# Kernel tuning notes

Measured on AMD Instinct MI355X. Metric: run time of the kernel, lower is better.

## Reference

```python
import jax, jax.numpy as jnp
import numpy as np

DCR = 8      # depth_channel_ratio
CLIP = 0.3   # clipping_ratio
ITER = 32    # iterative_num
EPS = 1e-6


def setup_inputs() -> dict:
    key = jax.random.key(0)
    k1, k2 = jax.random.split(key)
    B, C, H, W = 8, 128, 96, 320
    input_features = jax.random.normal(k1, (B, C, H, W), dtype=jnp.float32)
    dynamic_masks = jax.random.randint(k2, (B, H, W), 0, 2, dtype=jnp.int32)
    return {"input_features": input_features, "dynamic_masks": dynamic_masks}


def _channel_selection(x):
    # Select 2*(C//DCR) channels most similar to pseudo disparity/depth ramps.
    B, C, H, W = x.shape
    disp = jnp.linspace(0.1, 1.0, H, dtype=x.dtype)                      # (H,)
    disp_full = jnp.broadcast_to(disp[None, :, None], (B, H, W)).reshape(-1)  # (B*H*W,)
    depth_full = 1.0 - disp_full
    s = jax.nn.sigmoid(x).transpose(1, 0, 2, 3).reshape(C, -1)           # (C, B*H*W)
    sn = jnp.maximum(jnp.sqrt(jnp.sum(s * s, axis=-1)), EPS)             # (C,)

    def cos_sim(v):
        vn = jnp.maximum(jnp.sqrt(jnp.sum(v * v)), EPS)
        return (s @ v) / (sn * vn)                                       # (C,)

    nsel = C // DCR
    disp_idx = jnp.argsort(-cos_sim(disp_full))[:nsel]
    depth_idx = jnp.argsort(-cos_sim(depth_full))[:nsel]
    return jnp.concatenate([disp_idx, depth_idx])                        # (2*nsel,)


def _clip_norm(v, clip_ratio):
    # per-(batch,channel) max over spatial dims, scaled, zero->1, clamp to [0,1]
    m = jnp.max(v, axis=(2, 3), keepdims=True) * clip_ratio
    m = jnp.where(m == 0, jnp.ones_like(m), m)
    return jnp.clip(v / m, 0.0, 1.0)


def reference(input_features, dynamic_masks):
    B, C, H, W = input_features.shape
    idx = _channel_selection(input_features)
    sel = input_features[:, idx]                       # (B, ns, H, W)
    # mask resolution == feature resolution, so nearest resize is identity
    m = dynamic_masks.astype(input_features.dtype)[:, None]  # (B,1,H,W) broadcast over ns
    iters = int(ITER * H / dynamic_masks.shape[1])     # == ITER here (static)

    pad_bottom = lambda t: jnp.concatenate([t, t[:, :, -1:]], axis=2)
    prop0 = pad_bottom(sel)                            # (B, ns, H+1, W)

    def step(prop, _):
        core = m * prop[:, :, 1:] + (1.0 - m) * sel    # pull values up one row where masked
        return pad_bottom(core), None

    prop, _ = jax.lax.scan(step, prop0, None, length=iters)
    prop = prop[:, :, :-1]                             # (B, ns, H, W)

    w = _clip_norm(jnp.abs(prop - sel), CLIP)
    w = jnp.max(w, axis=1, keepdims=True)              # (B,1,H,W)
    refined = w * prop + (1.0 - w) * sel
    return input_features.at[:, idx].set(refined)
```

## Files before the change

### kernel.cpp

```cpp
#include <hip/hip_runtime.h>
#include <cstdint>
#include <cstddef>

#define BB 8
#define CC 128
#define HH 96
#define WW 320
#define HW (HH*WW)
#define NSEL 32
#define NSELH 16
#define K1CH 2
#define K4CH 8

typedef float f32x4 __attribute__((ext_vector_type(4)));

__device__ __forceinline__ float sigmoidf_(float x) {
  return __builtin_amdgcn_rcpf(1.0f + __expf(-x));
}

__global__ __launch_bounds__(256) void k_copy_reduce(
    const float* __restrict__ x, float* __restrict__ out,
    double* __restrict__ partials) {
  int t = threadIdx.x;
  int chunk = blockIdx.x & (K1CH-1);
  int bc = blockIdx.x >> 1;
  const f32x4* __restrict__ xi = (const f32x4*)(x + (size_t)bc * HW);
  f32x4* __restrict__ oi = (f32x4*)(out + (size_t)bc * HW);
  float tf = 0.0f, af = 0.0f, qf = 0.0f;
  #pragma unroll 1
  for (int outer = 0; outer < 3; ++outer) {
    int base = chunk*3840 + outer*1280;
    f32x4 v[5];
    #pragma unroll
    for (int u = 0; u < 5; u++) v[u] = xi[base + u*256 + t];
    __builtin_amdgcn_sched_barrier(0);
    #pragma unroll
    for (int u = 0; u < 5; u++) oi[base + u*256 + t] = v[u];
    #pragma unroll
    for (int u = 0; u < 5; u++) {
      int j = base + u*256 + t;
      int h = j / (WW/4);
      float d = 0.1f + (float)h * (0.9f/95.0f);
      float s0 = sigmoidf_(v[u].x), s1 = sigmoidf_(v[u].y);
      float s2 = sigmoidf_(v[u].z), s3 = sigmoidf_(v[u].w);
      float ts = (s0+s1)+(s2+s3);
      tf += ts;
      af += ts * d;
      qf += (s0*s0+s1*s1)+(s2*s2+s3*s3);
    }
  }
  __shared__ double sh[3][256];
  sh[0][t]=(double)tf; sh[1][t]=(double)af; sh[2][t]=(double)qf;
  __syncthreads();
  for (int ofs=128; ofs>0; ofs>>=1) {
    if (t < ofs) {
      sh[0][t]+=sh[0][t+ofs];
      sh[1][t]+=sh[1][t+ofs];
      sh[2][t]+=sh[2][t+ofs];
    }
    __syncthreads();
  }
  if (t==0) {
    int p = bc*K1CH + chunk;
    partials[p*3+0]=sh[0][0];
    partials[p*3+1]=sh[1][0];
    partials[p*3+2]=sh[2][0];
  }
}

__global__ __launch_bounds__(128) void k_select_runs(
    const double* __restrict__ partials, const int* __restrict__ mask,
    int* __restrict__ idx, uint8_t* __restrict__ kk) {
  int t = threadIdx.x;
  if (blockIdx.x == 0) {
    int c = t;
    double T=0.0, A=0.0, Q=0.0;
    for (int b=0;b<BB;b++) {
      for (int ch=0; ch<K1CH; ch++) {
        int p = (b*CC + c)*K1CH + ch;
        T += partials[p*3+0];
        A += partials[p*3+1];
        Q += partials[p*3+2];
      }
    }
    double sn = sqrt(Q); if (sn < 1e-6) sn = 1e-6;
    double c1 = A / sn;
    double c2 = (T - A) / sn;
    __shared__ double s1[CC], s2[CC];
    s1[c]=c1; s2[c]=c2;
    __syncthreads();
    int r1=0, r2=0;
    for (int j=0;j<CC;j++) {
      r1 += (s1[j] > c1) || (s1[j]==c1 && j<c);
      r2 += (s2[j] > c2) || (s2[j]==c2 && j<c);
    }
    if (r1 < NSELH) idx[r1] = c;
    if (r2 < NSELH) idx[NSELH + r2] = c;
  } else {
    int colid = (blockIdx.x - 1)*128 + t;
    int b = colid / WW;
    int w = colid - b*WW;
    const int* __restrict__ mcol = mask + (size_t)b*HW + w;
    unsigned long long lo=0ull, hi=0ull;
    #pragma unroll
    for (int h=0; h<64; ++h) lo |= (unsigned long long)(mcol[h*WW]!=0) << h;
    #pragma unroll
    for (int h=64; h<95; ++h) hi |= (unsigned long long)(mcol[h*WW]!=0) << (h-64);
    uint8_t* __restrict__ kcol = kk + (size_t)b*HW + w;
    #pragma unroll
    for (int h=0; h<96; ++h) {
      unsigned long long s;
      if (h == 0)      s = lo;
      else if (h < 64) s = (lo >> h) | (hi << (64-h));
      else             s = hi >> (h-64);
      int run = __builtin_ctzll(~s | (1ull<<33));
      kcol[h*WW] = (uint8_t)(run > 32 ? 32 : run);
    }
  }
}

__global__ __launch_bounds__(256) void k_maxdiff(
    const float* __restrict__ x, const int* __restrict__ idx,
    const uint8_t* __restrict__ kk, float* __restrict__ pmax) {
  int chunk = blockIdx.x & (K4CH-1);
  int bc32 = blockIdx.x >> 3;
  int b = bc32 >> 5;
  int c = bc32 & 31;
  int ic = idx[c];
  const float* __restrict__ base = x + ((size_t)b*CC + ic)*HW;
  const uint8_t* __restrict__ kb = kk + (size_t)b*HW;
  float mx = 0.0f;
  int lo = chunk * (HW/4/K4CH), hiend = lo + (HW/4/K4CH);
  for (int j = lo + threadIdx.x; j < hiend; j += 256) {
    f32x4 sel = ((const f32x4*)base)[j];
    uchar4 kv  = ((const uchar4*)kb)[j];
    int h = j / (WW/4);
    int w4 = (j - h*(WW/4))*4;
    float p0 = base[(h+(int)kv.x)*WW + w4+0];
    float p1 = base[(h+(int)kv.y)*WW + w4+1];
    float p2 = base[(h+(int)kv.z)*WW + w4+2];
    float p3 = base[(h+(int)kv.w)*WW + w4+3];
    mx = fmaxf(mx, fmaxf(fmaxf(fabsf(p0-sel.x), fabsf(p1-sel.y)),
                         fmaxf(fabsf(p2-sel.z), fabsf(p3-sel.w))));
  }
  __shared__ float sh[256];
  sh[threadIdx.x]=mx; __syncthreads();
  for (int ofs=128; ofs>0; ofs>>=1) {
    if ((int)threadIdx.x<ofs) sh[threadIdx.x]=fmaxf(sh[threadIdx.x], sh[threadIdx.x+ofs]);
    __syncthreads();
  }
  if (threadIdx.x==0) pmax[blockIdx.x] = sh[0];
}

__global__ __launch_bounds__(WW) void k_refine(
    const float* __restrict__ x, const int* __restrict__ idx,
    const uint8_t* __restrict__ kk, const float* __restrict__ pmax,
    float* __restrict__ out) {
  int bh = blockIdx.x;
  int b = bh / HH, h = bh - b*HH;
  int w = threadIdx.x;
  __shared__ int sidx[NSEL];
  __shared__ float smc[NSEL];
  if (threadIdx.x < NSEL) {
    int c = threadIdx.x;
    sidx[c] = idx[c];
    float m = 0.0f;
    #pragma unroll
    for (int ch=0; ch<K4CH; ch++) m = fmaxf(m, pmax[(b*NSEL + c)*K4CH + ch]);
    m *= 0.3f;
    if (m == 0.0f) m = 1.0f;
    smc[c] = m;
  }
  __syncthreads();
  int r = h + (int)kk[(size_t)bh*WW + w];
  float sel[NSEL], prop[NSEL];
  float wmax = 0.0f;
  #pragma unroll
  for (int c=0;c<NSEL;c++) {
    const float* __restrict__ base = x + ((size_t)b*CC + sidx[c])*HW;
    sel[c]  = base[h*WW + w];
    prop[c] = base[r*WW + w];
    float v = fabsf(prop[c]-sel[c]) / smc[c];
    wmax = fmaxf(wmax, fminf(v, 1.0f));
  }
  #pragma unroll
  for (int c=0;c<NSEL;c++) {
    float rf = wmax*prop[c] + (1.0f - wmax)*sel[c];
    out[((size_t)b*CC + sidx[c])*HW + h*WW + w] = rf;
  }
}

extern "C" void kernel_launch(void* const* d_in, const int* in_sizes, int n_in,
                              void* d_out, int out_size, void* d_ws, size_t ws_size,
                              hipStream_t stream) {
  const float* x   = (const float*)d_in[0];
  const int* mask  = (const int*)d_in[1];
  float* out       = (float*)d_out;

  char* ws = (char*)d_ws;
  double* partials = (double*)(ws);
  int*    idx      = (int*)(ws + 49152);
  float*  pmax     = (float*)(ws + 49152 + 128);
  uint8_t* kk      = (uint8_t*)(ws + 49152 + 128 + 8192);

  k_copy_reduce<<<BB*CC*K1CH, 256, 0, stream>>>(x, out, partials);
  k_select_runs<<<21, 128, 0, stream>>>(partials, mask, idx, kk);
  k_maxdiff<<<BB*NSEL*K4CH, 256, 0, stream>>>(x, idx, kk, pmax);
  k_refine<<<BB*HH, WW, 0, stream>>>(x, idx, kk, pmax, out);
}
```

Baseline: 95.72 us.

## Grid-stride copy-reduce with wave-level partial sums and separate plane reduction kernel

The copy-plus-sigmoid-statistics kernel moves from 2048 blocks each owning half a channel plane to a fixed 2048-block grid-stride loop over the whole tensor. Each wavefront reduces its partials with shuffles and writes float partials per step. A new kernel then sums those per-plane partials in double. The aim is a streaming access pattern and cheaper in-kernel reductions, paid for by an extra launch and float partial accumulation before the double sum.

```diff
diff --git a/kernel.cpp b/kernel.cpp
--- a/kernel.cpp
+++ b/kernel.cpp
@@ -9,8 +9,9 @@
 #define HW (HH*WW)
 #define NSEL 32
 #define NSELH 16
-#define K1CH 2
 #define K4CH 8
+#define GRID1 2048
+#define STEPS 15
 
 typedef float f32x4 __attribute__((ext_vector_type(4)));
 
@@ -18,70 +19,88 @@
   return __builtin_amdgcn_rcpf(1.0f + __expf(-x));
 }
 
+__device__ __forceinline__ float wred(float v) {
+  #pragma unroll
+  for (int m = 32; m >= 1; m >>= 1) v += __shfl_xor(v, m, 64);
+  return v;
+}
+
 __global__ __launch_bounds__(256) void k_copy_reduce(
     const float* __restrict__ x, float* __restrict__ out,
-    double* __restrict__ partials) {
+    float* __restrict__ wpart) {
   int t = threadIdx.x;
-  int chunk = blockIdx.x & (K1CH-1);
-  int bc = blockIdx.x >> 1;
-  const f32x4* __restrict__ xi = (const f32x4*)(x + (size_t)bc * HW);
-  f32x4* __restrict__ oi = (f32x4*)(out + (size_t)bc * HW);
-  float tf = 0.0f, af = 0.0f, qf = 0.0f;
+  int blk = blockIdx.x;
+  int wv = t >> 6;
+  const f32x4* __restrict__ xi = (const f32x4*)x;
+  f32x4* __restrict__ oi = (f32x4*)out;
   #pragma unroll 1
-  for (int outer = 0; outer < 3; ++outer) {
-    int base = chunk*3840 + outer*1280;
-    f32x4 v[5];
-    #pragma unroll
-    for (int u = 0; u < 5; u++) v[u] = xi[base + u*256 + t];
-    __builtin_amdgcn_sched_barrier(0);
-    #pragma unroll
-    for (int u = 0; u < 5; u++) oi[base + u*256 + t] = v[u];
-    #pragma unroll
-    for (int u = 0; u < 5; u++) {
-      int j = base + u*256 + t;
-      int h = j / (WW/4);
-      float d = 0.1f + (float)h * (0.9f/95.0f);
-      float s0 = sigmoidf_(v[u].x), s1 = sigmoidf_(v[u].y);
-      float s2 = sigmoidf_(v[u].z), s3 = sigmoidf_(v[u].w);
-      float ts = (s0+s1)+(s2+s3);
-      tf += ts;
-      af += ts * d;
-      qf += (s0*s0+s1*s1)+(s2*s2+s3*s3);
-    }
-  }
-  __shared__ double sh[3][256];
-  sh[0][t]=(double)tf; sh[1][t]=(double)af; sh[2][t]=(double)qf;
+  for (int s = 0; s < STEPS; ++s) {
+    int g = (s << 19) + blk*256 + t;
+    f32x4 v = xi[g];
+    oi[g] = v;
+    unsigned ip = (unsigned)g % 7680u;
+    int h = (int)(ip / 80u);
+    float d = 0.1f + (float)h * (0.9f/95.0f);
+    float s0 = sigmoidf_(v.x), s1 = sigmoidf_(v.y);
+    float s2 = sigmoidf_(v.z), s3 = sigmoidf_(v.w);
+    float ts = (s0+s1)+(s2+s3);
+    float qs = (s0*s0+s1*s1)+(s2*s2+s3*s3);
+    float tw = wred(ts);
+    float aw = wred(ts * d);
+    float qw = wred(qs);
+    if ((t & 63) == 0) {
+      int m = (s << 13) + (blk << 2) + wv;
+      wpart[m*3+0] = tw;
+      wpart[m*3+1] = aw;
+      wpart[m*3+2] = qw;
+    }
+  }
+}
+
+__global__ __launch_bounds__(128) void k_plane(
+    const float* __restrict__ wpart, double* __restrict__ planesums) {
+  int p = blockIdx.x;
+  int j = threadIdx.x;
+  double t0=0.0, t1=0.0, t2=0.0;
+  if (j < 120) {
+    int g0 = p*7680 + j*64;
+    int s  = g0 >> 19;
+    int r  = g0 & 524287;
+    int m  = (s << 13) + ((r >> 8) << 2) + ((r & 255) >> 6);
+    t0 = (double)wpart[m*3+0];
+    t1 = (double)wpart[m*3+1];
+    t2 = (double)wpart[m*3+2];
+  }
+  __shared__ double sh[3][128];
+  sh[0][j]=t0; sh[1][j]=t1; sh[2][j]=t2;
   __syncthreads();
-  for (int ofs=128; ofs>0; ofs>>=1) {
-    if (t < ofs) {
-      sh[0][t]+=sh[0][t+ofs];
-      sh[1][t]+=sh[1][t+ofs];
-      sh[2][t]+=sh[2][t+ofs];
+  for (int ofs=64; ofs>0; ofs>>=1) {
+    if (j < ofs) {
+      sh[0][j]+=sh[0][j+ofs];
+      sh[1][j]+=sh[1][j+ofs];
+      sh[2][j]+=sh[2][j+ofs];
     }
     __syncthreads();
   }
-  if (t==0) {
-    int p = bc*K1CH + chunk;
-    partials[p*3+0]=sh[0][0];
-    partials[p*3+1]=sh[1][0];
-    partials[p*3+2]=sh[2][0];
+  if (j==0) {
+    planesums[p*3+0]=sh[0][0];
+    planesums[p*3+1]=sh[1][0];
+    planesums[p*3+2]=sh[2][0];
   }
 }
 
 __global__ __launch_bounds__(128) void k_select_runs(
-    const double* __restrict__ partials, const int* __restrict__ mask,
+    const double* __restrict__ planesums, const int* __restrict__ mask,
     int* __restrict__ idx, uint8_t* __restrict__ kk) {
   int t = threadIdx.x;
   if (blockIdx.x == 0) {
     int c = t;
     double T=0.0, A=0.0, Q=0.0;
     for (int b=0;b<BB;b++) {
-      for (int ch=0; ch<K1CH; ch++) {
-        int p = (b*CC + c)*K1CH + ch;
-        T += partials[p*3+0];
-        A += partials[p*3+1];
-        Q += partials[p*3+2];
-      }
+      int p = b*CC + c;
+      T += planesums[p*3+0];
+      A += planesums[p*3+1];
+      Q += planesums[p*3+2];
     }
     double sn = sqrt(Q); if (sn < 1e-6) sn = 1e-6;
     double c1 = A / sn;
@@ -198,13 +217,15 @@
   float* out       = (float*)d_out;
 
   char* ws = (char*)d_ws;
-  double* partials = (double*)(ws);
-  int*    idx      = (int*)(ws + 49152);
-  float*  pmax     = (float*)(ws + 49152 + 128);
-  uint8_t* kk      = (uint8_t*)(ws + 49152 + 128 + 8192);
-
-  k_copy_reduce<<<BB*CC*K1CH, 256, 0, stream>>>(x, out, partials);
-  k_select_runs<<<21, 128, 0, stream>>>(partials, mask, idx, kk);
+  float*  wpart     = (float*)(ws);
+  double* planesums = (double*)(ws + 1474560);
+  int*    idx       = (int*)(ws + 1474560 + 24576);
+  float*  pmax      = (float*)(ws + 1474560 + 24576 + 128);
+  uint8_t* kk       = (uint8_t*)(ws + 1474560 + 24576 + 128 + 8192);
+
+  k_copy_reduce<<<GRID1, 256, 0, stream>>>(x, out, wpart);
+  k_plane<<<BB*CC, 128, 0, stream>>>(wpart, planesums);
+  k_select_runs<<<21, 128, 0, stream>>>(planesums, mask, idx, kk);
   k_maxdiff<<<BB*NSEL*K4CH, 256, 0, stream>>>(x, idx, kk, pmax);
   k_refine<<<BB*HH, WW, 0, stream>>>(x, idx, kk, pmax, out);
 }
```

Measured after the change: 99.07 us. 1.04x slower.

## Double-buffer copy-reduce loads through LDS with async global_load_lds

Applied to the files above, without the earlier changes.

Replaces register loads in the copy+sigmoid-reduction kernel with asynchronous global-to-LDS loads (16-byte global_load_lds) into a double-buffered shared array. The next iteration's chunk is prefetched while the current one is stored and reduced, with manual vmcnt waits. This aims to overlap HBM reads with compute and writes. In exchange it uses about 40KB of LDS per block, which lowers occupancy, and the hand-written waitcnt sequencing is fragile.

```diff
diff --git a/kernel.cpp b/kernel.cpp
--- a/kernel.cpp
+++ b/kernel.cpp
@@ -21,50 +21,71 @@
 __global__ __launch_bounds__(256) void k_copy_reduce(
     const float* __restrict__ x, float* __restrict__ out,
     double* __restrict__ partials) {
+  __shared__ float lbuf[2][5][4][256];
   int t = threadIdx.x;
+  int wv = t >> 6;
+  int lane = t & 63;
   int chunk = blockIdx.x & (K1CH-1);
   int bc = blockIdx.x >> 1;
-  const f32x4* __restrict__ xi = (const f32x4*)(x + (size_t)bc * HW);
-  f32x4* __restrict__ oi = (f32x4*)(out + (size_t)bc * HW);
-  float tf = 0.0f, af = 0.0f, qf = 0.0f;
+  const float* __restrict__ xp = x + (size_t)bc * HW;
+  f32x4* __restrict__ op = (f32x4*)(out + (size_t)bc * HW);
+  float tf = 0.f, af = 0.f, qf = 0.f;
+
+  #pragma unroll
+  for (int u = 0; u < 5; ++u) {
+    const float* g = xp + (size_t)(chunk*3840 + u*256 + t) * 4;
+    __builtin_amdgcn_global_load_lds(
+        (const __attribute__((address_space(1))) void*)g,
+        (__attribute__((address_space(3))) void*)&lbuf[0][u][wv][0], 16, 0, 0);
+  }
   #pragma unroll 1
   for (int outer = 0; outer < 3; ++outer) {
-    int base = chunk*3840 + outer*1280;
-    f32x4 v[5];
-    #pragma unroll
-    for (int u = 0; u < 5; u++) v[u] = xi[base + u*256 + t];
+    int buf = outer & 1;
+    if (outer < 2) {
+      #pragma unroll
+      for (int u = 0; u < 5; ++u) {
+        const float* g = xp + (size_t)(chunk*3840 + (outer+1)*1280 + u*256 + t) * 4;
+        __builtin_amdgcn_global_load_lds(
+            (const __attribute__((address_space(1))) void*)g,
+            (__attribute__((address_space(3))) void*)&lbuf[buf^1][u][wv][0], 16, 0, 0);
+      }
+    }
+    if (outer == 0)      asm volatile("s_waitcnt vmcnt(5)" ::: "memory");
+    else if (outer == 1) asm volatile("s_waitcnt vmcnt(10)" ::: "memory");
+    else                 asm volatile("s_waitcnt vmcnt(5)" ::: "memory");
     __builtin_amdgcn_sched_barrier(0);
     #pragma unroll
-    for (int u = 0; u < 5; u++) oi[base + u*256 + t] = v[u];
-    #pragma unroll
-    for (int u = 0; u < 5; u++) {
-      int j = base + u*256 + t;
-      int h = j / (WW/4);
+    for (int u = 0; u < 5; ++u) {
+      f32x4 v = *(const f32x4*)&lbuf[buf][u][wv][lane*4];
+      int j = chunk*3840 + outer*1280 + u*256 + t;
+      op[j] = v;
+      int h = j / 80;
       float d = 0.1f + (float)h * (0.9f/95.0f);
-      float s0 = sigmoidf_(v[u].x), s1 = sigmoidf_(v[u].y);
-      float s2 = sigmoidf_(v[u].z), s3 = sigmoidf_(v[u].w);
+      float s0 = sigmoidf_(v.x), s1 = sigmoidf_(v.y);
+      float s2 = sigmoidf_(v.z), s3 = sigmoidf_(v.w);
       float ts = (s0+s1)+(s2+s3);
       tf += ts;
       af += ts * d;
       qf += (s0*s0+s1*s1)+(s2*s2+s3*s3);
     }
   }
-  __shared__ double sh[3][256];
-  sh[0][t]=(double)tf; sh[1][t]=(double)af; sh[2][t]=(double)qf;
+  __syncthreads();
+  double* sh = (double*)&lbuf[0][0][0][0];
+  sh[0*256+t]=(double)tf; sh[1*256+t]=(double)af; sh[2*256+t]=(double)qf;
   __syncthreads();
   for (int ofs=128; ofs>0; ofs>>=1) {
     if (t < ofs) {
-      sh[0][t]+=sh[0][t+ofs];
-      sh[1][t]+=sh[1][t+ofs];
-      sh[2][t]+=sh[2][t+ofs];
+      sh[0*256+t]+=sh[0*256+t+ofs];
+      sh[1*256+t]+=sh[1*256+t+ofs];
+      sh[2*256+t]+=sh[2*256+t+ofs];
     }
     __syncthreads();
   }
   if (t==0) {
     int p = bc*K1CH + chunk;
-    partials[p*3+0]=sh[0][0];
-    partials[p*3+1]=sh[1][0];
-    partials[p*3+2]=sh[2][0];
+    partials[p*3+0]=sh[0];
+    partials[p*3+1]=sh[256];
+    partials[p*3+2]=sh[512];
   }
 }
 
```

Measured after the change: 95.60 us. No clear change (-0.1%).
